# Kernel optimization log

Hardware: AMD Instinct MI355X
Metric: run time of the kernel (lower is better)

## Reference

```python
import jax, jax.numpy as jnp
import numpy as np

DIM = 64          # d_model
D_INNER = 128     # 2 * DIM (mamba expand=2)
D_STATE = 16
D_CONV = 4
DT_RANK = 4       # ceil(DIM / 16)


def setup_inputs() -> dict:
    key = jax.random.key(0)
    ks = jax.random.split(key, 8)
    s = 0.05
    f32 = jnp.float32
    return {
        "x": jax.random.normal(ks[0], (2, DIM, 96, 96), f32),
        # GroupNorm(1, dim)
        "gn_gamma": jnp.ones((DIM,), f32),
        "gn_beta": jnp.zeros((DIM,), f32),
        # Mamba params
        "W_in": (jax.random.normal(ks[1], (2 * D_INNER, DIM), f32) * s),
        "b_in": jnp.zeros((2 * D_INNER,), f32),
        "conv_w": (jax.random.normal(ks[2], (D_INNER, 1, D_CONV), f32) * s),
        "conv_b": jnp.zeros((D_INNER,), f32),
        "W_xproj": (jax.random.normal(ks[3], (DT_RANK + 2 * D_STATE, D_INNER), f32) * s),
        "W_dt": (jax.random.normal(ks[4], (D_INNER, DT_RANK), f32) * s),
        "b_dt": jnp.full((D_INNER,), -4.6, f32),  # softplus(-4.6) ~ 0.01
        "A_log": jnp.log(jnp.broadcast_to(jnp.arange(1, D_STATE + 1, dtype=f32), (D_INNER, D_STATE))),
        "Dp": jnp.ones((D_INNER,), f32),
        "W_out": (jax.random.normal(ks[5], (DIM, D_INNER), f32) * s),
        "b_out": jnp.zeros((DIM,), f32),
        # proj: Conv2d(dim, dim, 1) + BatchNorm2d(dim) eval-mode + GELU
        "proj_w": (jax.random.normal(ks[6], (DIM, DIM), f32) * s),
        "proj_b": jnp.zeros((DIM,), f32),
        "bn_gamma": jnp.ones((DIM,), f32),
        "bn_beta": jnp.zeros((DIM,), f32),
        "bn_mean": jnp.zeros((DIM,), f32),
        "bn_var": jnp.ones((DIM,), f32),
    }


def _mamba(u, W_in, b_in, conv_w, conv_b, W_xproj, W_dt, b_dt, A_log, Dp, W_out, b_out):
    # u: [B, L, DIM]
    xz = u @ W_in.T + b_in                      # [B, L, 2*D_INNER]
    x, z = jnp.split(xz, 2, axis=-1)            # each [B, L, D_INNER]
    # depthwise causal conv over L
    xc = jnp.transpose(x, (0, 2, 1))            # [B, D_INNER, L]
    xc = jax.lax.conv_general_dilated(
        xc, conv_w, (1,), [(D_CONV - 1, 0)],
        dimension_numbers=("NCH", "OIH", "NCH"), feature_group_count=D_INNER)
    x = jax.nn.silu(jnp.transpose(xc, (0, 2, 1)) + conv_b)   # [B, L, D_INNER]
    # input-dependent dt, B, C
    dbc = x @ W_xproj.T                          # [B, L, DT_RANK + 2*D_STATE]
    dt = dbc[..., :DT_RANK]
    Bm = dbc[..., DT_RANK:DT_RANK + D_STATE]     # [B, L, D_STATE]
    Cm = dbc[..., DT_RANK + D_STATE:]            # [B, L, D_STATE]
    dt = jax.nn.softplus(dt @ W_dt.T + b_dt)     # [B, L, D_INNER]
    A = -jnp.exp(A_log)                          # [D_INNER, D_STATE]
    deltaA = jnp.exp(dt[..., None] * A)                          # [B, L, D_INNER, D_STATE]
    deltaBu = dt[..., None] * Bm[:, :, None, :] * x[..., None]   # [B, L, D_INNER, D_STATE]
    # parallel linear recurrence h_t = a_t * h_{t-1} + b_t, h_0 = 0
    def comb(e1, e2):
        a1, b1 = e1
        a2, b2 = e2
        return a1 * a2, a2 * b1 + b2
    _, h = jax.lax.associative_scan(comb, (deltaA, deltaBu), axis=1)
    y = jnp.einsum("blds,bls->bld", h, Cm) + x * Dp
    y = y * jax.nn.silu(z)
    return y @ W_out.T + b_out                   # [B, L, DIM]


def reference(x, gn_gamma, gn_beta, W_in, b_in, conv_w, conv_b, W_xproj, W_dt, b_dt,
              A_log, Dp, W_out, b_out, proj_w, proj_b, bn_gamma, bn_beta, bn_mean, bn_var):
    B, C, H, W = x.shape
    # GroupNorm(1, C): normalize over (C, H, W) per sample, biased var
    mu = x.mean(axis=(1, 2, 3), keepdims=True)
    var = x.var(axis=(1, 2, 3), keepdims=True)
    xn = (x - mu) / jnp.sqrt(var + 1e-5)
    xn = xn * gn_gamma[None, :, None, None] + gn_beta[None, :, None, None]
    xn = jnp.clip(xn, -10.0, 10.0)
    res = xn
    seq = jnp.transpose(xn, (0, 2, 3, 1)).reshape(B, H * W, C)
    y = _mamba(seq, W_in, b_in, conv_w, conv_b, W_xproj, W_dt, b_dt, A_log, Dp, W_out, b_out)
    y2d = jnp.transpose(y.reshape(B, H, W, C), (0, 3, 1, 2))
    # proj: 1x1 conv + eval BatchNorm + exact GELU
    p = jnp.einsum("oc,bchw->bohw", proj_w, y2d) + proj_b[None, :, None, None]
    p = (p - bn_mean[None, :, None, None]) / jnp.sqrt(bn_var[None, :, None, None] + 1e-5)
    p = p * bn_gamma[None, :, None, None] + bn_beta[None, :, None, None]
    p = jax.nn.gelu(p, approximate=False)
    return jnp.clip(res + p, -10.0, 10.0)
```

## Files before the change

### kernel.cpp

```cpp
#include <hip/hip_runtime.h>
#include <math.h>

#define DIMC 64
#define DIN  128
#define LSEQ 9216
#define NPB  (DIMC*LSEQ)
#define NCH  192
#define CTL  48
#define NCHAIN 4096

__device__ __forceinline__ float siluf(float v)    { return v / (1.f + __expf(-v)); }
__device__ __forceinline__ float softplusf(float v){ return (v > 20.f) ? v : log1pf(__expf(v)); }
__device__ __forceinline__ float clip10(float v)   { return fminf(10.f, fmaxf(-10.f, v)); }

__global__ void k_reduce(const float* __restrict__ x, float* __restrict__ sums) {
  int b = blockIdx.y;
  const float* xb = x + (size_t)b * NPB;
  float s = 0.f, s2 = 0.f;
  for (int i = blockIdx.x * blockDim.x + threadIdx.x; i < NPB; i += gridDim.x * blockDim.x) {
    float v = xb[i]; s += v; s2 = fmaf(v, v, s2);
  }
  __shared__ float l1[256], l2[256];
  int t = threadIdx.x;
  l1[t] = s; l2[t] = s2; __syncthreads();
  for (int off = 128; off > 0; off >>= 1) {
    if (t < off) { l1[t] += l1[t + off]; l2[t] += l2[t + off]; }
    __syncthreads();
  }
  if (t == 0) { atomicAdd(&sums[2*b], l1[0]); atomicAdd(&sums[2*b+1], l2[0]); }
}

__global__ void k_norm(const float* __restrict__ x, const float* __restrict__ gam,
                       const float* __restrict__ bet, const float* __restrict__ sums,
                       float* __restrict__ seq, float* __restrict__ res) {
  int b = blockIdx.y, l0 = blockIdx.x * 64;
  float mean = sums[2*b] * (1.f / NPB);
  float var  = sums[2*b+1] * (1.f / NPB) - mean * mean;
  float inv  = rsqrtf(var + 1e-5f);
  __shared__ float tile[64][65];
  int t = threadIdx.x;
  int lr = t & 63, cg = t >> 6;
  #pragma unroll
  for (int i = 0; i < 16; i++) {
    int c = i * 4 + cg;
    size_t idx = ((size_t)(b * DIMC + c)) * LSEQ + l0 + lr;
    float v = x[idx];
    v = (v - mean) * inv * gam[c] + bet[c];
    v = clip10(v);
    res[idx] = v;
    tile[c][lr] = v;
  }
  __syncthreads();
  int cc = t & 63, lg = t >> 6;
  #pragma unroll
  for (int i = 0; i < 16; i++) {
    int l = i * 4 + lg;
    seq[((size_t)(b * LSEQ + l0 + l)) * DIMC + cc] = tile[cc][l];
  }
}

__global__ void k_prep(const float* __restrict__ W_in, const float* __restrict__ proj_w,
                       const float* __restrict__ W_out, const float* __restrict__ b_out,
                       const float* __restrict__ proj_b, const float* __restrict__ W_xproj,
                       const float* __restrict__ W_dt, const float* __restrict__ b_dt,
                       float* __restrict__ Wt, float* __restrict__ Mt, float* __restrict__ bp,
                       float* __restrict__ Wbt, float* __restrict__ bbig) {
  int i = blockIdx.x * 256 + threadIdx.x;
  if (i < 16384) {
    int k = i >> 8, c = i & 255;
    Wt[i] = W_in[c * 64 + k];
    return;
  }
  int j = i - 16384;
  if (j < 8192) {
    int d = j >> 6, o = j & 63;
    float a = 0.f;
    for (int c = 0; c < 64; c++) a = fmaf(proj_w[o * 64 + c], W_out[c * DIN + d], a);
    Mt[j] = a;
    return;
  }
  int k2 = j - 8192;
  if (k2 < 64) {
    float a = proj_b[k2];
    for (int c = 0; c < 64; c++) a = fmaf(proj_w[k2 * 64 + c], b_out[c], a);
    bp[k2] = a;
    return;
  }
  int m = j - 8256;
  if (m < 20480) {
    int k = m / 160, c = m - k * 160;
    float v;
    if (c < 128) {
      v = 0.f;
      #pragma unroll
      for (int r = 0; r < 4; r++) v = fmaf(W_dt[c * 4 + r], W_xproj[r * DIN + k], v);
    } else {
      v = W_xproj[(c - 124) * DIN + k];
    }
    Wbt[m] = v;
    return;
  }
  int c3 = m - 20480;
  if (c3 < 160) bbig[c3] = (c3 < 128) ? b_dt[c3] : 0.f;
}

__global__ void k_inproj_conv(const float* __restrict__ seq, const float* __restrict__ Wt,
                              const float* __restrict__ b_in, const float* __restrict__ conv_w,
                              const float* __restrict__ conv_b,
                              float* __restrict__ xs, float* __restrict__ zo) {
  int row0 = blockIdx.x * 16;
  int l0 = row0 % LSEQ;
  int t = threadIdx.x;
  __shared__ float sq[19 * 64];
  for (int i = t; i < 19 * 16; i += 256) {
    int r = i >> 4, k4 = i & 15;
    int rr = row0 - 3 + r; if (rr < 0) rr = 0;
    *(float4*)(sq + r * 64 + k4 * 4) = *(const float4*)(seq + (size_t)rr * DIMC + k4 * 4);
  }
  __syncthreads();

  int c = t;
  float bi = b_in[c];
  float a[19];
  #pragma unroll
  for (int r = 0; r < 19; r++) a[r] = bi;
  const float4* sq4 = (const float4*)sq;
  #pragma unroll 4
  for (int k4 = 0; k4 < 16; k4++) {
    float w0 = Wt[(k4 * 4 + 0) * 256 + c];
    float w1 = Wt[(k4 * 4 + 1) * 256 + c];
    float w2 = Wt[(k4 * 4 + 2) * 256 + c];
    float w3 = Wt[(k4 * 4 + 3) * 256 + c];
    #pragma unroll
    for (int r = 0; r < 19; r++) {
      float4 v = sq4[r * 16 + k4];
      a[r] = fmaf(w0, v.x, a[r]);
      a[r] = fmaf(w1, v.y, a[r]);
      a[r] = fmaf(w2, v.z, a[r]);
      a[r] = fmaf(w3, v.w, a[r]);
    }
  }
  if (c < DIN) {
    if (l0 == 0) { a[0] = 0.f; a[1] = 0.f; a[2] = 0.f; }
    float4 cw = *(const float4*)(conv_w + c * 4);
    float cb = conv_b[c];
    #pragma unroll
    for (int i = 0; i < 16; i++) {
      float v = cb;
      v = fmaf(a[i + 0], cw.x, v);
      v = fmaf(a[i + 1], cw.y, v);
      v = fmaf(a[i + 2], cw.z, v);
      v = fmaf(a[i + 3], cw.w, v);
      xs[(size_t)(row0 + i) * DIN + c] = siluf(v);
    }
  } else {
    int cz = c - DIN;
    #pragma unroll
    for (int i = 0; i < 16; i++) zo[(size_t)(row0 + i) * DIN + cz] = a[i + 3];
  }
}

__global__ void k_xproj(const float* __restrict__ xs, const float* __restrict__ Wbt,
                        const float* __restrict__ bbig,
                        float* __restrict__ dt, float* __restrict__ Bm, float* __restrict__ Cm) {
  int row0 = blockIdx.x * 16;
  int t = threadIdx.x;
  __shared__ float xt[16 * DIN];
  for (int i = t; i < 16 * 32; i += 320) {
    int r = i >> 5, k4 = i & 31;
    *(float4*)(xt + r * DIN + k4 * 4) = *(const float4*)(xs + (size_t)(row0 + r) * DIN + k4 * 4);
  }
  __syncthreads();

  int c = (t < 160) ? t : t - 160;
  int rbase = (t < 160) ? 0 : 8;
  float acc[8];
  float bb = bbig[c];
  #pragma unroll
  for (int r = 0; r < 8; r++) acc[r] = bb;
  const float4* xt4 = (const float4*)(xt + rbase * DIN);
  #pragma unroll 2
  for (int k4 = 0; k4 < 32; k4++) {
    float w0 = Wbt[(k4 * 4 + 0) * 160 + c];
    float w1 = Wbt[(k4 * 4 + 1) * 160 + c];
    float w2 = Wbt[(k4 * 4 + 2) * 160 + c];
    float w3 = Wbt[(k4 * 4 + 3) * 160 + c];
    #pragma unroll
    for (int r = 0; r < 8; r++) {
      float4 v = xt4[r * 32 + k4];
      acc[r] = fmaf(w0, v.x, acc[r]);
      acc[r] = fmaf(w1, v.y, acc[r]);
      acc[r] = fmaf(w2, v.z, acc[r]);
      acc[r] = fmaf(w3, v.w, acc[r]);
    }
  }
  if (c < 128) {
    #pragma unroll
    for (int r = 0; r < 8; r++)
      dt[(size_t)(row0 + rbase + r) * DIN + c] = softplusf(acc[r]);
  } else if (c < 144) {
    #pragma unroll
    for (int r = 0; r < 8; r++)
      Bm[(size_t)(row0 + rbase + r) * 16 + (c - 128)] = acc[r];
  } else {
    #pragma unroll
    for (int r = 0; r < 8; r++)
      Cm[(size_t)(row0 + rbase + r) * 16 + (c - 144)] = acc[r];
  }
}

__global__ void __launch_bounds__(512) k_scanA(
    const float* __restrict__ dt, const float* __restrict__ Bmat,
    const float* __restrict__ xs, const float* __restrict__ A_log,
    float* __restrict__ Ap, float* __restrict__ Bg) {
  int chunk = blockIdx.x, b = blockIdx.y;
  int t = threadIdx.x;
  int d = t >> 2, q = t & 3;
  const float* al = A_log + d * 16 + q * 4;
  float a0 = -__expf(al[0]), a1 = -__expf(al[1]);
  float a2 = -__expf(al[2]), a3 = -__expf(al[3]);
  size_t base = (size_t)b * LSEQ + (size_t)chunk * CTL;
  const float* dtp = dt + base * DIN + d;
  const float* xsp = xs + base * DIN + d;
  const float4* bp4 = (const float4*)(Bmat + base * 16 + q * 4);
  float h0 = 0.f, h1 = 0.f, h2 = 0.f, h3 = 0.f;
  float p0 = 1.f, p1 = 1.f, p2 = 1.f, p3 = 1.f;
  #pragma unroll 4
  for (int i = 0; i < CTL; i++) {
    float dtv = dtp[(size_t)i * DIN];
    float xv  = xsp[(size_t)i * DIN];
    float4 bA = bp4[i * 4];
    float u = dtv * xv;
    float e;
    e = __expf(dtv * a0); h0 = fmaf(e, h0, u * bA.x); p0 *= e;
    e = __expf(dtv * a1); h1 = fmaf(e, h1, u * bA.y); p1 *= e;
    e = __expf(dtv * a2); h2 = fmaf(e, h2, u * bA.z); p2 *= e;
    e = __expf(dtv * a3); h3 = fmaf(e, h3, u * bA.w); p3 *= e;
  }
  size_t idx = (size_t)chunk * NCHAIN + (size_t)(b * DIN + d) * 16 + q * 4;
  *(float4*)(Ap + idx) = make_float4(p0, p1, p2, p3);
  *(float4*)(Bg + idx) = make_float4(h0, h1, h2, h3);
}

__global__ void k_scanB(const float* __restrict__ Ap, const float* __restrict__ Bg,
                        float* __restrict__ hinit) {
  int chain = blockIdx.x * 64 + threadIdx.x;
  float h = 0.f;
  for (int c = 0; c < NCH; c++) {
    size_t idx = (size_t)c * NCHAIN + chain;
    hinit[idx] = h;
    h = fmaf(Ap[idx], h, Bg[idx]);
  }
}

__global__ void __launch_bounds__(512) k_scanC(
    const float* __restrict__ dt, const float* __restrict__ Bmat,
    const float* __restrict__ Cmat, const float* __restrict__ xs,
    const float* __restrict__ z, const float* __restrict__ A_log,
    const float* __restrict__ Dp, const float* __restrict__ hinit,
    float* __restrict__ y) {
  int chunk = blockIdx.x, b = blockIdx.y;
  int t = threadIdx.x;
  int d = t >> 2, q = t & 3;
  const float* al = A_log + d * 16 + q * 4;
  float a0 = -__expf(al[0]), a1 = -__expf(al[1]);
  float a2 = -__expf(al[2]), a3 = -__expf(al[3]);
  float dp = Dp[d];
  size_t base = (size_t)b * LSEQ + (size_t)chunk * CTL;
  const float* dtp = dt + base * DIN + d;
  const float* xsp = xs + base * DIN + d;
  const float* zp  = z  + base * DIN + d;
  float* yp        = y  + base * DIN + d;
  const float4* bp4 = (const float4*)(Bmat + base * 16 + q * 4);
  const float4* cp4 = (const float4*)(Cmat + base * 16 + q * 4);
  size_t idx = (size_t)chunk * NCHAIN + (size_t)(b * DIN + d) * 16 + q * 4;
  float4 hv = *(const float4*)(hinit + idx);
  float h0 = hv.x, h1 = hv.y, h2 = hv.z, h3 = hv.w;
  #pragma unroll 2
  for (int i = 0; i < CTL; i++) {
    float dtv = dtp[(size_t)i * DIN];
    float xv  = xsp[(size_t)i * DIN];
    float4 bA = bp4[i * 4];
    float4 cA = cp4[i * 4];
    float u = dtv * xv;
    float e, p;
    e = __expf(dtv * a0); h0 = fmaf(e, h0, u * bA.x); p  = h0 * cA.x;
    e = __expf(dtv * a1); h1 = fmaf(e, h1, u * bA.y); p  = fmaf(h1, cA.y, p);
    e = __expf(dtv * a2); h2 = fmaf(e, h2, u * bA.z); p  = fmaf(h2, cA.z, p);
    e = __expf(dtv * a3); h3 = fmaf(e, h3, u * bA.w); p  = fmaf(h3, cA.w, p);
    p += __shfl_xor(p, 1);
    p += __shfl_xor(p, 2);
    if (q == 0) {
      float zv = zp[(size_t)i * DIN];
      yp[(size_t)i * DIN] = (p + xv * dp) * siluf(zv);
    }
  }
}

__global__ void k_out(const float* __restrict__ y, const float* __restrict__ Mt,
                      const float* __restrict__ bp, const float* __restrict__ bn_g,
                      const float* __restrict__ bn_bt, const float* __restrict__ bn_m,
                      const float* __restrict__ bn_v, const float* __restrict__ res,
                      float* __restrict__ out) {
  int b = blockIdx.y, l0 = blockIdx.x * 64;
  int t = threadIdx.x;
  int c = t & 63, lg = t >> 6;
  __shared__ float tile[64][65];
  float acc[16];
  float bpc = bp[c];
  #pragma unroll
  for (int i = 0; i < 16; i++) acc[i] = bpc;
  const float* yb = y + ((size_t)b * LSEQ + l0 + lg * 16) * DIN;
  #pragma unroll 4
  for (int d = 0; d < DIN; d++) {
    float m = Mt[d * 64 + c];
    #pragma unroll
    for (int i = 0; i < 16; i++) acc[i] = fmaf(m, yb[i * DIN + d], acc[i]);
  }
  float g = bn_g[c], bt = bn_bt[c], mu = bn_m[c];
  float iv = rsqrtf(bn_v[c] + 1e-5f);
  #pragma unroll
  for (int i = 0; i < 16; i++) {
    float a = (acc[i] - mu) * iv * g + bt;
    a = 0.5f * a * (1.f + erff(a * 0.70710678118654752f));
    tile[c][lg * 16 + i] = a;
  }
  __syncthreads();
  int l = t & 63, cg = t >> 6;
  #pragma unroll
  for (int i = 0; i < 16; i++) {
    int cc = cg * 16 + i;
    size_t idx = ((size_t)(b * DIMC + cc)) * LSEQ + l0 + l;
    out[idx] = clip10(res[idx] + tile[cc][l]);
  }
}

extern "C" void kernel_launch(void* const* d_in, const int* in_sizes, int n_in,
                              void* d_out, int out_size, void* d_ws, size_t ws_size,
                              hipStream_t stream) {
  const float* x       = (const float*)d_in[0];
  const float* gn_g    = (const float*)d_in[1];
  const float* gn_b    = (const float*)d_in[2];
  const float* W_in    = (const float*)d_in[3];
  const float* b_in    = (const float*)d_in[4];
  const float* conv_w  = (const float*)d_in[5];
  const float* conv_b  = (const float*)d_in[6];
  const float* W_xproj = (const float*)d_in[7];
  const float* W_dt    = (const float*)d_in[8];
  const float* b_dt    = (const float*)d_in[9];
  const float* A_log   = (const float*)d_in[10];
  const float* Dp      = (const float*)d_in[11];
  const float* W_out   = (const float*)d_in[12];
  const float* b_out   = (const float*)d_in[13];
  const float* proj_w  = (const float*)d_in[14];
  const float* proj_b  = (const float*)d_in[15];
  const float* bn_g    = (const float*)d_in[16];
  const float* bn_bt   = (const float*)d_in[17];
  const float* bn_m    = (const float*)d_in[18];
  const float* bn_v    = (const float*)d_in[19];

  float* ws = (float*)d_ws;
  float* sums = ws;
  float* seq  = ws + 64;
  float* res  = seq + 1179648;
  float* ybuf = res + 1179648;
  float* zbuf = ybuf + 2359296;
  float* xsb  = zbuf + 2359296;
  float* dtb  = xsb + 2359296;
  float* Bmb  = dtb + 2359296;
  float* Cmb  = Bmb + 294912;
  float* Wt   = Cmb + 294912;
  float* Mt   = Wt + 16384;
  float* bp   = Mt + 8192;
  float* Wbt  = bp + 64;
  float* bbig = Wbt + 20480;
  float* Bgb  = bbig + 160;
  float* hib  = Bgb + 786432;
  float* Apb  = seq;

  hipMemsetAsync(sums, 0, 64 * sizeof(float), stream);

  k_reduce<<<dim3(256, 2), 256, 0, stream>>>(x, sums);
  k_prep<<<177, 256, 0, stream>>>(W_in, proj_w, W_out, b_out, proj_b, W_xproj, W_dt, b_dt,
                                  Wt, Mt, bp, Wbt, bbig);
  k_norm<<<dim3(144, 2), 256, 0, stream>>>(x, gn_g, gn_b, sums, seq, res);
  k_inproj_conv<<<1152, 256, 0, stream>>>(seq, Wt, b_in, conv_w, conv_b, xsb, zbuf);
  k_xproj<<<1152, 320, 0, stream>>>(xsb, Wbt, bbig, dtb, Bmb, Cmb);
  k_scanA<<<dim3(NCH, 2), 512, 0, stream>>>(dtb, Bmb, xsb, A_log, Apb, Bgb);
  k_scanB<<<64, 64, 0, stream>>>(Apb, Bgb, hib);
  k_scanC<<<dim3(NCH, 2), 512, 0, stream>>>(dtb, Bmb, Cmb, xsb, zbuf, A_log, Dp, hib, ybuf);
  k_out<<<dim3(144, 2), 256, 0, stream>>>(ybuf, Mt, bp, bn_g, bn_bt, bn_m, bn_v, res,
                                          (float*)d_out);
}
```

Baseline: 284.3 us.

## Fuse in-projection/conv with x-projection kernel and retile output projection

```diff
diff --git a/kernel.cpp b/kernel.cpp
--- a/kernel.cpp
+++ b/kernel.cpp
@@ -10,7 +10,7 @@
 #define NCHAIN 4096
 
 __device__ __forceinline__ float siluf(float v)    { return v / (1.f + __expf(-v)); }
-__device__ __forceinline__ float softplusf(float v){ return (v > 20.f) ? v : log1pf(__expf(v)); }
+__device__ __forceinline__ float softplusf(float v){ return (v > 15.f) ? v : __logf(1.f + __expf(v)); }
 __device__ __forceinline__ float clip10(float v)   { return fminf(10.f, fmaxf(-10.f, v)); }
 
 __global__ void k_reduce(const float* __restrict__ x, float* __restrict__ sums) {
@@ -62,9 +62,9 @@
 __global__ void k_prep(const float* __restrict__ W_in, const float* __restrict__ proj_w,
                        const float* __restrict__ W_out, const float* __restrict__ b_out,
                        const float* __restrict__ proj_b, const float* __restrict__ W_xproj,
-                       const float* __restrict__ W_dt, const float* __restrict__ b_dt,
+                       const float* __restrict__ W_dt,
                        float* __restrict__ Wt, float* __restrict__ Mt, float* __restrict__ bp,
-                       float* __restrict__ Wbt, float* __restrict__ bbig) {
+                       float* __restrict__ Wbtd, float* __restrict__ Wbc) {
   int i = blockIdx.x * 256 + threadIdx.x;
   if (i < 16384) {
     int k = i >> 8, c = i & 255;
@@ -87,31 +87,33 @@
     return;
   }
   int m = j - 8256;
-  if (m < 20480) {
-    int k = m / 160, c = m - k * 160;
-    float v;
-    if (c < 128) {
-      v = 0.f;
-      #pragma unroll
-      for (int r = 0; r < 4; r++) v = fmaf(W_dt[c * 4 + r], W_xproj[r * DIN + k], v);
-    } else {
-      v = W_xproj[(c - 124) * DIN + k];
-    }
-    Wbt[m] = v;
+  if (m < 16384) {
+    int k = m >> 7, c = m & 127;
+    float v = 0.f;
+    #pragma unroll
+    for (int r = 0; r < 4; r++) v = fmaf(W_dt[c * 4 + r], W_xproj[r * DIN + k], v);
+    Wbtd[m] = v;
     return;
   }
-  int c3 = m - 20480;
-  if (c3 < 160) bbig[c3] = (c3 < 128) ? b_dt[c3] : 0.f;
-}
-
-__global__ void k_inproj_conv(const float* __restrict__ seq, const float* __restrict__ Wt,
-                              const float* __restrict__ b_in, const float* __restrict__ conv_w,
-                              const float* __restrict__ conv_b,
-                              float* __restrict__ xs, float* __restrict__ zo) {
+  int m2 = m - 16384;
+  if (m2 < 4096) {
+    int k = m2 >> 5, jj = m2 & 31;
+    Wbc[m2] = W_xproj[(4 + jj) * DIN + k];
+  }
+}
+
+__global__ void __launch_bounds__(256) k_mid(
+    const float* __restrict__ seq, const float* __restrict__ Wt,
+    const float* __restrict__ b_in, const float* __restrict__ conv_w,
+    const float* __restrict__ conv_b, const float* __restrict__ Wbtd,
+    const float* __restrict__ Wbc, const float* __restrict__ b_dt,
+    float* __restrict__ xs, float* __restrict__ zo, float* __restrict__ dt,
+    float* __restrict__ Bm, float* __restrict__ Cm) {
   int row0 = blockIdx.x * 16;
   int l0 = row0 % LSEQ;
   int t = threadIdx.x;
   __shared__ float sq[19 * 64];
+  __shared__ float xt[16 * DIN];
   for (int i = t; i < 19 * 16; i += 256) {
     int r = i >> 4, k4 = i & 15;
     int rr = row0 - 3 + r; if (rr < 0) rr = 0;
@@ -119,93 +121,99 @@
   }
   __syncthreads();
 
-  int c = t;
-  float bi = b_in[c];
-  float a[19];
-  #pragma unroll
-  for (int r = 0; r < 19; r++) a[r] = bi;
-  const float4* sq4 = (const float4*)sq;
-  #pragma unroll 4
-  for (int k4 = 0; k4 < 16; k4++) {
-    float w0 = Wt[(k4 * 4 + 0) * 256 + c];
-    float w1 = Wt[(k4 * 4 + 1) * 256 + c];
-    float w2 = Wt[(k4 * 4 + 2) * 256 + c];
-    float w3 = Wt[(k4 * 4 + 3) * 256 + c];
+  {
+    int c = t;
+    float bi = b_in[c];
+    float a[19];
     #pragma unroll
-    for (int r = 0; r < 19; r++) {
-      float4 v = sq4[r * 16 + k4];
-      a[r] = fmaf(w0, v.x, a[r]);
-      a[r] = fmaf(w1, v.y, a[r]);
-      a[r] = fmaf(w2, v.z, a[r]);
-      a[r] = fmaf(w3, v.w, a[r]);
-    }
-  }
-  if (c < DIN) {
-    if (l0 == 0) { a[0] = 0.f; a[1] = 0.f; a[2] = 0.f; }
-    float4 cw = *(const float4*)(conv_w + c * 4);
-    float cb = conv_b[c];
+    for (int r = 0; r < 19; r++) a[r] = bi;
+    const float4* sq4 = (const float4*)sq;
+    #pragma unroll 4
+    for (int k4 = 0; k4 < 16; k4++) {
+      float w0 = Wt[(k4 * 4 + 0) * 256 + c];
+      float w1 = Wt[(k4 * 4 + 1) * 256 + c];
+      float w2 = Wt[(k4 * 4 + 2) * 256 + c];
+      float w3 = Wt[(k4 * 4 + 3) * 256 + c];
+      #pragma unroll
+      for (int r = 0; r < 19; r++) {
+        float4 v = sq4[r * 16 + k4];
+        a[r] = fmaf(w0, v.x, a[r]);
+        a[r] = fmaf(w1, v.y, a[r]);
+        a[r] = fmaf(w2, v.z, a[r]);
+        a[r] = fmaf(w3, v.w, a[r]);
+      }
+    }
+    if (c < DIN) {
+      if (l0 == 0) { a[0] = 0.f; a[1] = 0.f; a[2] = 0.f; }
+      float4 cw = *(const float4*)(conv_w + c * 4);
+      float cb = conv_b[c];
+      #pragma unroll
+      for (int i = 0; i < 16; i++) {
+        float v = cb;
+        v = fmaf(a[i + 0], cw.x, v);
+        v = fmaf(a[i + 1], cw.y, v);
+        v = fmaf(a[i + 2], cw.z, v);
+        v = fmaf(a[i + 3], cw.w, v);
+        float sv = siluf(v);
+        xs[(size_t)(row0 + i) * DIN + c] = sv;
+        xt[i * DIN + c] = sv;
+      }
+    } else {
+      int cz = c - DIN;
+      #pragma unroll
+      for (int i = 0; i < 16; i++) zo[(size_t)(row0 + i) * DIN + cz] = a[i + 3];
+    }
+  }
+  __syncthreads();
+
+  {
+    int cd = t & 127, rb = (t >> 7) * 8;
+    float acc[8];
+    float bb = b_dt[cd];
     #pragma unroll
-    for (int i = 0; i < 16; i++) {
-      float v = cb;
-      v = fmaf(a[i + 0], cw.x, v);
-      v = fmaf(a[i + 1], cw.y, v);
-      v = fmaf(a[i + 2], cw.z, v);
-      v = fmaf(a[i + 3], cw.w, v);
-      xs[(size_t)(row0 + i) * DIN + c] = siluf(v);
-    }
-  } else {
-    int cz = c - DIN;
-    #pragma unroll
-    for (int i = 0; i < 16; i++) zo[(size_t)(row0 + i) * DIN + cz] = a[i + 3];
-  }
-}
-
-__global__ void k_xproj(const float* __restrict__ xs, const float* __restrict__ Wbt,
-                        const float* __restrict__ bbig,
-                        float* __restrict__ dt, float* __restrict__ Bm, float* __restrict__ Cm) {
-  int row0 = blockIdx.x * 16;
-  int t = threadIdx.x;
-  __shared__ float xt[16 * DIN];
-  for (int i = t; i < 16 * 32; i += 320) {
-    int r = i >> 5, k4 = i & 31;
-    *(float4*)(xt + r * DIN + k4 * 4) = *(const float4*)(xs + (size_t)(row0 + r) * DIN + k4 * 4);
-  }
-  __syncthreads();
-
-  int c = (t < 160) ? t : t - 160;
-  int rbase = (t < 160) ? 0 : 8;
-  float acc[8];
-  float bb = bbig[c];
-  #pragma unroll
-  for (int r = 0; r < 8; r++) acc[r] = bb;
-  const float4* xt4 = (const float4*)(xt + rbase * DIN);
-  #pragma unroll 2
-  for (int k4 = 0; k4 < 32; k4++) {
-    float w0 = Wbt[(k4 * 4 + 0) * 160 + c];
-    float w1 = Wbt[(k4 * 4 + 1) * 160 + c];
-    float w2 = Wbt[(k4 * 4 + 2) * 160 + c];
-    float w3 = Wbt[(k4 * 4 + 3) * 160 + c];
-    #pragma unroll
-    for (int r = 0; r < 8; r++) {
-      float4 v = xt4[r * 32 + k4];
-      acc[r] = fmaf(w0, v.x, acc[r]);
-      acc[r] = fmaf(w1, v.y, acc[r]);
-      acc[r] = fmaf(w2, v.z, acc[r]);
-      acc[r] = fmaf(w3, v.w, acc[r]);
-    }
-  }
-  if (c < 128) {
+    for (int r = 0; r < 8; r++) acc[r] = bb;
+    const float4* xt4 = (const float4*)(xt + rb * DIN);
+    #pragma unroll 2
+    for (int k4 = 0; k4 < 32; k4++) {
+      float w0 = Wbtd[(k4 * 4 + 0) * 128 + cd];
+      float w1 = Wbtd[(k4 * 4 + 1) * 128 + cd];
+      float w2 = Wbtd[(k4 * 4 + 2) * 128 + cd];
+      float w3 = Wbtd[(k4 * 4 + 3) * 128 + cd];
+      #pragma unroll
+      for (int r = 0; r < 8; r++) {
+        float4 v = xt4[r * 32 + k4];
+        acc[r] = fmaf(w0, v.x, acc[r]);
+        acc[r] = fmaf(w1, v.y, acc[r]);
+        acc[r] = fmaf(w2, v.z, acc[r]);
+        acc[r] = fmaf(w3, v.w, acc[r]);
+      }
+    }
     #pragma unroll
     for (int r = 0; r < 8; r++)
-      dt[(size_t)(row0 + rbase + r) * DIN + c] = softplusf(acc[r]);
-  } else if (c < 144) {
-    #pragma unroll
-    for (int r = 0; r < 8; r++)
-      Bm[(size_t)(row0 + rbase + r) * 16 + (c - 128)] = acc[r];
-  } else {
-    #pragma unroll
-    for (int r = 0; r < 8; r++)
-      Cm[(size_t)(row0 + rbase + r) * 16 + (c - 144)] = acc[r];
+      dt[(size_t)(row0 + rb + r) * DIN + cd] = softplusf(acc[r]);
+  }
+
+  {
+    int cb = t & 31, rg = t >> 5;
+    float a0 = 0.f, a1 = 0.f;
+    const float4* x0 = (const float4*)(xt + (rg * 2 + 0) * DIN);
+    const float4* x1 = (const float4*)(xt + (rg * 2 + 1) * DIN);
+    #pragma unroll 2
+    for (int k4 = 0; k4 < 32; k4++) {
+      float w0 = Wbc[(k4 * 4 + 0) * 32 + cb];
+      float w1 = Wbc[(k4 * 4 + 1) * 32 + cb];
+      float w2 = Wbc[(k4 * 4 + 2) * 32 + cb];
+      float w3 = Wbc[(k4 * 4 + 3) * 32 + cb];
+      float4 v0 = x0[k4], v1 = x1[k4];
+      a0 = fmaf(w0, v0.x, a0); a0 = fmaf(w1, v0.y, a0);
+      a0 = fmaf(w2, v0.z, a0); a0 = fmaf(w3, v0.w, a0);
+      a1 = fmaf(w0, v1.x, a1); a1 = fmaf(w1, v1.y, a1);
+      a1 = fmaf(w2, v1.z, a1); a1 = fmaf(w3, v1.w, a1);
+    }
+    size_t r0 = (size_t)row0 + rg * 2;
+    float* dst = (cb < 16) ? (Bm + r0 * 16 + cb) : (Cm + r0 * 16 + (cb - 16));
+    dst[0]  = a0;
+    dst[16] = a1;
   }
 }
 
@@ -297,41 +305,51 @@
   }
 }
 
-__global__ void k_out(const float* __restrict__ y, const float* __restrict__ Mt,
-                      const float* __restrict__ bp, const float* __restrict__ bn_g,
-                      const float* __restrict__ bn_bt, const float* __restrict__ bn_m,
-                      const float* __restrict__ bn_v, const float* __restrict__ res,
-                      float* __restrict__ out) {
-  int b = blockIdx.y, l0 = blockIdx.x * 64;
-  int t = threadIdx.x;
-  int c = t & 63, lg = t >> 6;
-  __shared__ float tile[64][65];
-  float acc[16];
+__global__ void __launch_bounds__(256) k_out(
+    const float* __restrict__ y, const float* __restrict__ Mt,
+    const float* __restrict__ bp, const float* __restrict__ bn_g,
+    const float* __restrict__ bn_bt, const float* __restrict__ bn_m,
+    const float* __restrict__ bn_v, const float* __restrict__ res,
+    float* __restrict__ out) {
+  int b = blockIdx.y, l0 = blockIdx.x * 32;
+  int t = threadIdx.x;
+  int c = t & 63, g = t >> 6;
+  __shared__ float tile[64 * 33];
+  float acc[8];
   float bpc = bp[c];
   #pragma unroll
-  for (int i = 0; i < 16; i++) acc[i] = bpc;
-  const float* yb = y + ((size_t)b * LSEQ + l0 + lg * 16) * DIN;
+  for (int i = 0; i < 8; i++) acc[i] = bpc;
+  const float* yb = y + ((size_t)b * LSEQ + l0 + g * 8) * DIN;
   #pragma unroll 4
-  for (int d = 0; d < DIN; d++) {
-    float m = Mt[d * 64 + c];
+  for (int d4 = 0; d4 < 32; d4++) {
+    float m0 = Mt[(d4 * 4 + 0) * 64 + c];
+    float m1 = Mt[(d4 * 4 + 1) * 64 + c];
+    float m2 = Mt[(d4 * 4 + 2) * 64 + c];
+    float m3 = Mt[(d4 * 4 + 3) * 64 + c];
     #pragma unroll
-    for (int i = 0; i < 16; i++) acc[i] = fmaf(m, yb[i * DIN + d], acc[i]);
-  }
-  float g = bn_g[c], bt = bn_bt[c], mu = bn_m[c];
+    for (int i = 0; i < 8; i++) {
+      float4 v = *(const float4*)(yb + (size_t)i * DIN + d4 * 4);
+      acc[i] = fmaf(m0, v.x, acc[i]);
+      acc[i] = fmaf(m1, v.y, acc[i]);
+      acc[i] = fmaf(m2, v.z, acc[i]);
+      acc[i] = fmaf(m3, v.w, acc[i]);
+    }
+  }
+  float gg = bn_g[c], bt = bn_bt[c], mu = bn_m[c];
   float iv = rsqrtf(bn_v[c] + 1e-5f);
   #pragma unroll
-  for (int i = 0; i < 16; i++) {
-    float a = (acc[i] - mu) * iv * g + bt;
+  for (int i = 0; i < 8; i++) {
+    float a = (acc[i] - mu) * iv * gg + bt;
     a = 0.5f * a * (1.f + erff(a * 0.70710678118654752f));
-    tile[c][lg * 16 + i] = a;
+    tile[c * 33 + g * 8 + i] = a;
   }
   __syncthreads();
-  int l = t & 63, cg = t >> 6;
+  int l = t & 31, cg = t >> 5;
   #pragma unroll
-  for (int i = 0; i < 16; i++) {
-    int cc = cg * 16 + i;
+  for (int i = 0; i < 8; i++) {
+    int cc = cg * 8 + i;
     size_t idx = ((size_t)(b * DIMC + cc)) * LSEQ + l0 + l;
-    out[idx] = clip10(res[idx] + tile[cc][l]);
+    out[idx] = clip10(res[idx] + tile[cc * 33 + l]);
   }
 }
 
@@ -372,23 +390,23 @@
   float* Wt   = Cmb + 294912;
   float* Mt   = Wt + 16384;
   float* bp   = Mt + 8192;
-  float* Wbt  = bp + 64;
-  float* bbig = Wbt + 20480;
-  float* Bgb  = bbig + 160;
+  float* Wbtd = bp + 64;
+  float* Wbc  = Wbtd + 16384;
+  float* Bgb  = Wbc + 4096;
   float* hib  = Bgb + 786432;
   float* Apb  = seq;
 
   hipMemsetAsync(sums, 0, 64 * sizeof(float), stream);
 
   k_reduce<<<dim3(256, 2), 256, 0, stream>>>(x, sums);
-  k_prep<<<177, 256, 0, stream>>>(W_in, proj_w, W_out, b_out, proj_b, W_xproj, W_dt, b_dt,
-                                  Wt, Mt, bp, Wbt, bbig);
+  k_prep<<<177, 256, 0, stream>>>(W_in, proj_w, W_out, b_out, proj_b, W_xproj, W_dt,
+                                  Wt, Mt, bp, Wbtd, Wbc);
   k_norm<<<dim3(144, 2), 256, 0, stream>>>(x, gn_g, gn_b, sums, seq, res);
-  k_inproj_conv<<<1152, 256, 0, stream>>>(seq, Wt, b_in, conv_w, conv_b, xsb, zbuf);
-  k_xproj<<<1152, 320, 0, stream>>>(xsb, Wbt, bbig, dtb, Bmb, Cmb);
+  k_mid<<<1152, 256, 0, stream>>>(seq, Wt, b_in, conv_w, conv_b, Wbtd, Wbc, b_dt,
+                                  xsb, zbuf, dtb, Bmb, Cmb);
   k_scanA<<<dim3(NCH, 2), 512, 0, stream>>>(dtb, Bmb, xsb, A_log, Apb, Bgb);
   k_scanB<<<64, 64, 0, stream>>>(Apb, Bgb, hib);
   k_scanC<<<dim3(NCH, 2), 512, 0, stream>>>(dtb, Bmb, Cmb, xsb, zbuf, A_log, Dp, hib, ybuf);
-  k_out<<<dim3(144, 2), 256, 0, stream>>>(ybuf, Mt, bp, bn_g, bn_bt, bn_m, bn_v, res,
+  k_out<<<dim3(288, 2), 256, 0, stream>>>(ybuf, Mt, bp, bn_g, bn_bt, bn_m, bn_v, res,
                                           (float*)d_out);
 }
```

Measured after the change: 267.3 us. -6.0%, faster.
